# Optimization experiments

Measured on AMD Instinct MI355X. Metric: run time of the kernel, lower is better.

Reference implementation:

```python
import jax, jax.numpy as jnp
import numpy as np

N_HEADS = 16
NEG_BIG = float(-2**32 + 1)  # value the original writes into masked positions


def setup_inputs() -> dict:
    key = jax.random.key(0)
    ks = jax.random.split(key, 5)
    B, T, D = 64, 256, 1024
    s = 1.0 / np.sqrt(D)
    return {
        "x": jax.random.normal(ks[0], (B, T, D), jnp.float32),
        "pos_emb": jax.random.normal(ks[1], (T, D), jnp.float32),
        "Wq": jax.random.normal(ks[2], (D, D), jnp.float32) * s,
        "Wk": jax.random.normal(ks[3], (D, D), jnp.float32) * s,
        "Wv": jax.random.normal(ks[4], (D, D), jnp.float32) * s,
    }


def reference(x, pos_emb, Wq, Wk, Wv):
    B, T, D = x.shape
    H = N_HEADS
    dh = D // H
    # add position embeddings (same arange positions for every batch row)
    temporal = x + pos_emb[None, :T, :]            # [B, T, D]
    q = temporal @ Wq                              # [B, T, D]
    k = temporal @ Wk
    v = temporal @ Wv
    # chunk along feature dim into H heads, concatenate along batch dim -> [H*B, T, dh]
    def split_heads(t):
        return jnp.concatenate(jnp.split(t, H, axis=2), axis=0)
    q_, k_, v_ = split_heads(q), split_heads(k), split_heads(v)
    scores = jnp.einsum('btd,bsd->bts', q_, k_) / jnp.sqrt(jnp.asarray(T, x.dtype))  # [H*B, T, T]
    # original masks the LOWER triangle (tril > 0 -> padding), faithful to source
    tril = jnp.tril(jnp.ones((T, T), x.dtype))
    scores = jnp.where(tril > 0, jnp.asarray(NEG_BIG, x.dtype), scores)
    # original applies softmax over dim=0 (the batch*head axis), faithful to source
    probs = jax.nn.softmax(scores, axis=0)         # [H*B, T, T]
    out = jnp.einsum('bts,bsd->btd', probs, v_)    # [H*B, T, dh]
    # merge heads back: chunk along batch dim, concatenate along feature dim
    out = jnp.concatenate(jnp.split(out, H, axis=0), axis=-1)  # [B, T, D]
    return out
```

## Files before the change

kernel.cpp:

```cpp
#include <hip/hip_runtime.h>

constexpr int SEQ = 256;
constexpr int DIM = 1024;
constexpr float SCALE = 0.0625f;

typedef __attribute__((ext_vector_type(8))) short bf16x8;
typedef __attribute__((ext_vector_type(4))) float f32x4;
typedef unsigned short ushort_t;
typedef unsigned int uint_t;

__device__ __forceinline__ void gld_lds16(const void* g, void* l) {
  __builtin_amdgcn_global_load_lds(
      (const __attribute__((address_space(1))) unsigned int*)g,
      (__attribute__((address_space(3))) unsigned int*)l, 16, 0, 0);
}

__device__ __forceinline__ ushort_t f2bf(float f) {
  uint_t u = __float_as_uint(f);
  return (ushort_t)((u + 0x7fffu + ((u >> 16) & 1u)) >> 16);
}

__device__ __forceinline__ float bf2f(ushort_t h) {
  return __uint_as_float(((uint_t)h) << 16);
}

__global__ __launch_bounds__(256)
void prep_pack(const float* __restrict__ x, const float* __restrict__ pos,
               const float* __restrict__ Wq, const float* __restrict__ Wk,
               const float* __restrict__ Wv,
               ushort_t* __restrict__ Ab, ushort_t* __restrict__ Bp) {
  const int bid = (int)blockIdx.x;
  if (bid < 8192) {
    const size_t idx = ((size_t)bid * 256 + threadIdx.x) * 8;
    const int m = (int)(idx >> 10), k = (int)(idx & 1023);
    float4 x0 = *(const float4*)(x + idx);
    float4 x1 = *(const float4*)(x + idx + 4);
    const float* pp = pos + ((size_t)(m & 255) << 10) + k;
    float4 p0 = *(const float4*)pp;
    float4 p1 = *(const float4*)(pp + 4);
    uint_t w0 = (uint_t)f2bf(x0.x + p0.x) | ((uint_t)f2bf(x0.y + p0.y) << 16);
    uint_t w1 = (uint_t)f2bf(x0.z + p0.z) | ((uint_t)f2bf(x0.w + p0.w) << 16);
    uint_t w2 = (uint_t)f2bf(x1.x + p1.x) | ((uint_t)f2bf(x1.y + p1.y) << 16);
    uint_t w3 = (uint_t)f2bf(x1.z + p1.z) | ((uint_t)f2bf(x1.w + p1.w) << 16);
    *(uint4*)&Ab[idx] = make_uint4(w0, w1, w2, w3);
  } else {
    const int pid = bid - 8192;
    const int z = pid >> 9;
    const int rem = pid & 511;
    const int by = rem >> 2, bx = rem & 3;
    const float* W = (z == 0) ? Wq : (z == 1) ? Wk : Wv;
    const int n  = bx * 256 + threadIdx.x;
    const int k8 = by * 8;
    uint_t h[8];
#pragma unroll
    for (int i = 0; i < 8; ++i) h[i] = f2bf(W[(size_t)(k8 + i) * DIM + n]);
    uint_t hp[4];
#pragma unroll
    for (int j = 0; j < 4; ++j) hp[j] = h[2 * j] | (h[2 * j + 1] << 16);
    const int np = z * 1024 + n;
    const int nb = np >> 8, nl = np & 255;
    const int kc = k8 >> 6, kk = k8 & 63;
    size_t base = (((size_t)nb * 16 + kc) * 256 + nl) * 64 + kk;
    *(uint4*)&Bp[base] = make_uint4(hp[0], hp[1], hp[2], hp[3]);
  }
}

__global__ __launch_bounds__(512, 2)
void qkv_mfma(const ushort_t* __restrict__ Ab, const ushort_t* __restrict__ Bp,
              ushort_t* __restrict__ q_bf, ushort_t* __restrict__ k_bf,
              ushort_t* __restrict__ vT_bf) {
  const int id = (int)blockIdx.x;
  const int q8 = id >> 3;
  const int nb = q8 % 12;
  const int mb = (id & 7) * 8 + q8 / 12;
  const int tid = (int)threadIdx.x;
  const int wave = tid >> 6, lane = tid & 63;
  const int wm = wave >> 2, wn = wave & 3;
  const int l15 = lane & 15, quad = lane >> 4;

  __shared__ ushort_t smem[65536];

  const int r8 = lane >> 3;
  const int lc8 = ((lane & 7) ^ r8) * 8;
  const size_t a_row = ((size_t)(mb * 256 + wave * 8 + r8)) << 10;
  const size_t b_row = ((size_t)((nb * 16) * 256 + wave * 8 + r8)) << 6;
  const int wb = wave * 512;

#define SA(q, tt, c) gld_lds16(Ab + a_row + ((size_t)(q) << 16) + (size_t)(tt) * 64 + lc8, \
                               smem + (c) * 32768 + (q) * 4096 + wb)
#define SB(q, tt, c) gld_lds16(Bp + b_row + (size_t)(tt) * 16384 + (q) * 4096 + lc8, \
                               smem + (c) * 32768 + 16384 + (q) * 4096 + wb)

  const int swz = l15 & 7;
  const int cko0 = (quad ^ swz) * 8;
  const int cko1 = ((4 + quad) ^ swz) * 8;
  const int arow0 = (wm * 128 + l15) * 64;
  const int brow0 = (wn * 64 + l15) * 64;

  f32x4 acc[8][4] = {};
  bf16x8 af[4][2], bf[4][2];

#define LDA_II(IH, ii) do { \
    const int ro = arow0 + ((IH) * 64 + (ii) * 16) * 64; \
    af[ii][0] = *(const bf16x8*)&Ac[ro + cko0]; \
    af[ii][1] = *(const bf16x8*)&Ac[ro + cko1]; } while (0)
#define LDB_J(J) do { const int ro = brow0 + (J) * 1024; \
    bf[J][0] = *(const bf16x8*)&Bc[ro + cko0]; \
    bf[J][1] = *(const bf16x8*)&Bc[ro + cko1]; } while (0)
#define MMQ(IH, II0, II1, J0) do { \
    _Pragma("unroll") for (int ks = 0; ks < 2; ++ks) \
    _Pragma("unroll") for (int ii = (II0); ii < (II1); ++ii) \
    _Pragma("unroll") for (int jj = 0; jj < 2; ++jj) \
      acc[(IH) * 4 + ii][(J0) + jj] = __builtin_amdgcn_mfma_f32_16x16x32_bf16( \
          af[ii][ks], bf[(J0) + jj][ks], acc[(IH) * 4 + ii][(J0) + jj], 0, 0, 0); \
    } while (0)

  SA(0, 0, 0); SA(2, 0, 0); SB(0, 0, 0); SB(1, 0, 0); SB(2, 0, 0); SB(3, 0, 0);
  SA(1, 0, 0); SA(3, 0, 0);
  SB(0, 1, 1); SB(1, 1, 1); SA(0, 1, 1); SA(2, 1, 1);
  asm volatile("s_waitcnt vmcnt(6)" ::: "memory");
  __builtin_amdgcn_s_barrier();

  for (int t = 0; t < 16; ++t) {
    const int cur = t & 1, nxt = cur ^ 1;
    const int tn  = (t < 15) ? t + 1 : 15;
    const int tn2 = (t < 14) ? t + 2 : 15;
    const ushort_t* Ac = &smem[cur * 32768];
    const ushort_t* Bc = Ac + 16384;
    LDA_II(0, 0); LDA_II(0, 1); LDA_II(0, 2); LDA_II(0, 3);
    LDB_J(0); LDB_J(1);
    SB(2, tn, nxt); SB(3, tn, nxt);
    __builtin_amdgcn_s_barrier();
    LDB_J(2); LDB_J(3);
    SA(1, tn, nxt); SA(3, tn, nxt);
    asm volatile("s_waitcnt lgkmcnt(4)" ::: "memory");
    __builtin_amdgcn_s_setprio(1);
    MMQ(0, 0, 4, 0);
    __builtin_amdgcn_s_setprio(0);
    asm volatile("s_waitcnt vmcnt(8)" ::: "memory");
    __builtin_amdgcn_s_barrier();
    asm volatile("s_waitcnt lgkmcnt(0)" ::: "memory");
    __builtin_amdgcn_s_setprio(1);
    MMQ(0, 0, 2, 2);
    __builtin_amdgcn_s_setprio(0);
    LDA_II(1, 0); LDA_II(1, 1);
    __builtin_amdgcn_s_setprio(1);
    MMQ(0, 2, 4, 2);
    __builtin_amdgcn_s_setprio(0);
    LDA_II(1, 2); LDA_II(1, 3);
    __builtin_amdgcn_s_barrier();
    SB(0, tn2, cur); SB(1, tn2, cur);
    asm volatile("s_waitcnt lgkmcnt(0)" ::: "memory");
    __builtin_amdgcn_s_setprio(1);
    MMQ(1, 0, 4, 2);
    __builtin_amdgcn_s_setprio(0);
    __builtin_amdgcn_s_barrier();
    SA(0, tn2, cur); SA(2, tn2, cur);
    __builtin_amdgcn_s_setprio(1);
    MMQ(1, 0, 4, 0);
    __builtin_amdgcn_s_setprio(0);
    asm volatile("s_waitcnt vmcnt(6)" ::: "memory");
    __builtin_amdgcn_s_barrier();
  }

  asm volatile("s_waitcnt vmcnt(0)" ::: "memory");
  const int wq = nb >> 2;
  const int h  = (nb & 3) * 4 + wn;
  if (wq < 2) {
    ushort_t* base = ((wq == 0) ? q_bf : k_bf) + (size_t)(mb * 16 + h) * (SEQ * 64);
    const int tb = wm * 128 + quad * 4;
#pragma unroll
    for (int i = 0; i < 8; ++i)
#pragma unroll
      for (int j = 0; j < 4; ++j) {
        const int d = j * 16 + l15;
#pragma unroll
        for (int r = 0; r < 4; ++r)
          base[(size_t)(tb + i * 16 + r) * 64 + d] = f2bf(acc[i][j][r]);
      }
  } else {
    __builtin_amdgcn_s_barrier();
    ushort_t* L = &smem[wave * 4608];
    ushort_t* vbase = vT_bf + (size_t)(mb * 16 + h) * (64 * SEQ) + wm * 128;
    const int tc = (lane & 7) * 8;
#pragma unroll
    for (int g = 0; g < 2; ++g) {
#pragma unroll
      for (int ii = 0; ii < 4; ++ii)
#pragma unroll
        for (int j = 0; j < 4; ++j) {
          f32x4 v = acc[g * 4 + ii][j];
          uint_t lo = (uint_t)f2bf(v[0]) | ((uint_t)f2bf(v[1]) << 16);
          uint_t hi = (uint_t)f2bf(v[2]) | ((uint_t)f2bf(v[3]) << 16);
          *(uint2*)&L[(j * 16 + l15) * 72 + ii * 16 + quad * 4] = make_uint2(lo, hi);
        }
#pragma unroll
      for (int u = 0; u < 8; ++u) {
        const int d = u * 8 + r8;
        uint4 val = *(const uint4*)&L[d * 72 + tc];
        *(uint4*)&vbase[(size_t)d * SEQ + g * 64 + tc] = val;
      }
    }
  }
#undef SA
#undef SB
#undef LDA_II
#undef LDB_J
#undef MMQ
}

__global__ __launch_bounds__(256)
void stats_mfma(const ushort_t* __restrict__ qb, const ushort_t* __restrict__ kb,
                float* __restrict__ part_l) {
  const int p = blockIdx.x, g = blockIdx.y;
  int tt, ss;
  if (p < 4) { tt = p; ss = p; }
  else {
    const int idx = p - 4;
    tt = (idx < 3) ? 0 : (idx < 5) ? 1 : 2;
    ss = (idx < 3) ? idx + 1 : (idx < 5) ? idx - 1 : 3;
  }
  const bool diag = (p < 4);
  const int tid = threadIdx.x, wave = tid >> 6, lane = tid & 63;
  const int l15 = lane & 15, quad = lane >> 4;

  __shared__ __attribute__((aligned(16))) float red[4][64 * 68];

  f32x4 lacc[4][4] = {};

  for (int i4 = 0; i4 < 8; ++i4) {
    const int bp = g * 32 + wave * 8 + i4;
    const int bh = (bp & 63) * 16 + (bp >> 6);
    const ushort_t* qt = qb + (size_t)bh * (SEQ * 64) + (size_t)(tt * 64) * 64;
    const ushort_t* kt = kb + (size_t)bh * (SEQ * 64) + (size_t)(ss * 64) * 64;
    bf16x8 aq[4][2], bk[4][2];
#pragma unroll
    for (int m = 0; m < 4; ++m)
#pragma unroll
      for (int ks = 0; ks < 2; ++ks) {
        aq[m][ks] = *(const bf16x8*)&qt[(m * 16 + l15) * 64 + ks * 32 + quad * 8];
        bk[m][ks] = *(const bf16x8*)&kt[(m * 16 + l15) * 64 + ks * 32 + quad * 8];
      }
    f32x4 sf[4][4] = {};
#pragma unroll
    for (int ks = 0; ks < 2; ++ks)
#pragma unroll
      for (int m = 0; m < 4; ++m)
#pragma unroll
        for (int n = 0; n < 4; ++n)
          sf[m][n] = __builtin_amdgcn_mfma_f32_16x16x32_bf16(aq[m][ks], bk[n][ks], sf[m][n], 0, 0, 0);
#pragma unroll
    for (int m = 0; m < 4; ++m)
#pragma unroll
      for (int n = 0; n < 4; ++n)
#pragma unroll
        for (int r = 0; r < 4; ++r) {
          float e = __expf(sf[m][n][r] * SCALE);
          if (diag) {
            const int t = tt * 64 + m * 16 + quad * 4 + r;
            const int s = ss * 64 + n * 16 + l15;
            e = (s > t) ? e : 1.0f;
          }
          lacc[m][n][r] += e;
        }
  }
  float* R = red[wave];
#pragma unroll
  for (int m = 0; m < 4; ++m)
#pragma unroll
    for (int r = 0; r < 4; ++r) {
      const int row = m * 16 + quad * 4 + r;
#pragma unroll
      for (int n = 0; n < 4; ++n)
        R[row * 68 + n * 16 + l15] = lacc[m][n][r];
    }
  __syncthreads();
  const int trow = tid >> 2, c0 = (tid & 3) * 16;
  const float* r0 = &red[0][trow * 68 + c0];
  const float* r1 = &red[1][trow * 68 + c0];
  const float* r2 = &red[2][trow * 68 + c0];
  const float* r3 = &red[3][trow * 68 + c0];
  float* pl = part_l + (size_t)g * (SEQ * SEQ) + (size_t)(tt * 64 + trow) * SEQ + ss * 64 + c0;
#pragma unroll
  for (int c = 0; c < 16; c += 4) {
    float4 s0 = *(const float4*)&r0[c];
    float4 s1 = *(const float4*)&r1[c];
    float4 s2 = *(const float4*)&r2[c];
    float4 s3 = *(const float4*)&r3[c];
    float4 o;
    o.x = (s0.x + s1.x) + (s2.x + s3.x);
    o.y = (s0.y + s1.y) + (s2.y + s3.y);
    o.z = (s0.z + s1.z) + (s2.z + s3.z);
    o.w = (s0.w + s1.w) + (s2.w + s3.w);
    *(float4*)&pl[c] = o;
  }
}

__global__ __launch_bounds__(256)
void merge_kernel(const float* __restrict__ part_l, float* __restrict__ inv_lT) {
  const int i = blockIdx.x * 256 + threadIdx.x;
  const int t = i >> 8, s = i & 255;
  float invv;
  if (s <= t) invv = 1.0f / 1024.0f;
  else {
    const float* p = part_l + i;
    float a0 = 0.f, a1 = 0.f, a2 = 0.f, a3 = 0.f,
          a4 = 0.f, a5 = 0.f, a6 = 0.f, a7 = 0.f;
    for (int g = 0; g < 32; g += 8) {
      const float* q = p + ((size_t)g << 16);
      a0 += q[0ull << 16]; a1 += q[1ull << 16]; a2 += q[2ull << 16]; a3 += q[3ull << 16];
      a4 += q[4ull << 16]; a5 += q[5ull << 16]; a6 += q[6ull << 16]; a7 += q[7ull << 16];
    }
    invv = 1.0f / (((a0 + a1) + (a2 + a3)) + ((a4 + a5) + (a6 + a7)));
  }
  inv_lT[s * SEQ + t] = invv;
}

__global__ __launch_bounds__(256)
void pv_mfma(const ushort_t* __restrict__ qb, const ushort_t* __restrict__ kb,
             const ushort_t* __restrict__ vtb, const float* __restrict__ inv_lT,
             float* __restrict__ out) {
  const int bh = blockIdx.x;
  const int b = bh >> 4, h = bh & 15;
  const int tid = threadIdx.x, wave = tid >> 6, lane = tid & 63;
  const int l15 = lane & 15, quad = lane >> 4;
  const int t0 = wave * 64;

  __shared__ ushort_t Plds[4][64][72];
  __shared__ float csumL[4][64];
  ushort_t (*Pw)[72] = Plds[wave];

  const ushort_t* qq = qb + (size_t)bh * (SEQ * 64);
  const ushort_t* kk = kb + (size_t)bh * (SEQ * 64);
  const ushort_t* vv = vtb + (size_t)bh * (64 * SEQ);

  {
    const int d = lane;
    const ushort_t* vr = vv + (size_t)d * SEQ + wave * 64;
    float s = 0.f;
#pragma unroll
    for (int j = 0; j < 8; ++j) {
      bf16x8 v8 = *(const bf16x8*)&vr[j * 8];
#pragma unroll
      for (int e = 0; e < 8; ++e) s += bf2f((ushort_t)v8[e]);
    }
    csumL[wave][d] = s;
  }

  bf16x8 qf[4][2];
#pragma unroll
  for (int nt = 0; nt < 4; ++nt)
#pragma unroll
    for (int ks = 0; ks < 2; ++ks)
      qf[nt][ks] = *(const bf16x8*)&qq[(t0 + nt * 16 + l15) * 64 + ks * 32 + quad * 8];

  __syncthreads();

  f32x4 o[4][4] = {};

  for (int sc = wave; sc < 4; ++sc) {
    bf16x8 kf[4][2];
#pragma unroll
    for (int ms = 0; ms < 4; ++ms)
#pragma unroll
      for (int ks = 0; ks < 2; ++ks)
        kf[ms][ks] = *(const bf16x8*)&kk[(sc * 64 + ms * 16 + l15) * 64 + ks * 32 + quad * 8];
    f32x4 sf[4][4] = {};
#pragma unroll
    for (int ks = 0; ks < 2; ++ks)
#pragma unroll
      for (int ms = 0; ms < 4; ++ms)
#pragma unroll
        for (int nt = 0; nt < 4; ++nt)
          sf[ms][nt] = __builtin_amdgcn_mfma_f32_16x16x32_bf16(kf[ms][ks], qf[nt][ks], sf[ms][nt], 0, 0, 0);
    const bool dg = (sc == wave);
    const int t = t0 + l15;
#pragma unroll
    for (int ms = 0; ms < 4; ++ms)
#pragma unroll
      for (int nt = 0; nt < 4; ++nt) {
        const int sb = sc * 64 + ms * 16 + quad * 4;
        const int tc = t + nt * 16;
        ushort_t pb[4];
#pragma unroll
        for (int r = 0; r < 4; ++r) {
          const int s = sb + r;
          float e = __expf(sf[ms][nt][r] * SCALE);
          if (dg) e = (s > tc) ? e : 1.0f;
          pb[r] = f2bf(e * inv_lT[(size_t)s * SEQ + tc]);
        }
        uint_t lo = (uint_t)pb[0] | ((uint_t)pb[1] << 16);
        uint_t hi = (uint_t)pb[2] | ((uint_t)pb[3] << 16);
        *(uint2*)&Pw[nt * 16 + l15][ms * 16 + quad * 4] = make_uint2(lo, hi);
      }

    bf16x8 vf[4][2], pf[4][2];
#pragma unroll
    for (int nd = 0; nd < 4; ++nd)
#pragma unroll
      for (int ks = 0; ks < 2; ++ks)
        vf[nd][ks] = *(const bf16x8*)&vv[(nd * 16 + l15) * SEQ + sc * 64 + ks * 32 + quad * 8];
#pragma unroll
    for (int mt = 0; mt < 4; ++mt)
#pragma unroll
      for (int ks = 0; ks < 2; ++ks)
        pf[mt][ks] = *(const bf16x8*)&Pw[mt * 16 + l15][ks * 32 + quad * 8];
#pragma unroll
    for (int ks = 0; ks < 2; ++ks)
#pragma unroll
      for (int mt = 0; mt < 4; ++mt)
#pragma unroll
        for (int nd = 0; nd < 4; ++nd)
          o[mt][nd] = __builtin_amdgcn_mfma_f32_16x16x32_bf16(pf[mt][ks], vf[nd][ks], o[mt][nd], 0, 0, 0);
  }

#pragma unroll
  for (int nd = 0; nd < 4; ++nd) {
    const int d = nd * 16 + l15;
    float pref = 0.f;
    for (int w2 = 0; w2 < wave; ++w2) pref += csumL[w2][d];
    const float cc = pref * (1.0f / 1024.0f);
#pragma unroll
    for (int mt = 0; mt < 4; ++mt)
#pragma unroll
      for (int r = 0; r < 4; ++r)
        o[mt][nd][r] += cc;
  }

  float* ob = out + (size_t)b * SEQ * DIM + h * 64;
#pragma unroll
  for (int mt = 0; mt < 4; ++mt)
#pragma unroll
    for (int r = 0; r < 4; ++r) {
      const int t = t0 + mt * 16 + quad * 4 + r;
#pragma unroll
      for (int nd = 0; nd < 4; ++nd)
        ob[(size_t)t * DIM + nd * 16 + l15] = o[mt][nd][r];
    }
}

extern "C" void kernel_launch(void* const* d_in, const int* in_sizes, int n_in,
                              void* d_out, int out_size, void* d_ws, size_t ws_size,
                              hipStream_t stream) {
  const float* x   = (const float*)d_in[0];
  const float* pos = (const float*)d_in[1];
  const float* Wq  = (const float*)d_in[2];
  const float* Wk  = (const float*)d_in[3];
  const float* Wv  = (const float*)d_in[4];
  float* out = (float*)d_out;

  ushort_t* Ab = (ushort_t*)d_out;
  ushort_t* Bp = (ushort_t*)((char*)d_out + 33554432);

  char* W = (char*)d_ws;
  ushort_t* q_bf   = (ushort_t*)(W);
  ushort_t* k_bf   = (ushort_t*)(W + 33554432);
  ushort_t* vT_bf  = (ushort_t*)(W + 67108864);
  float*    part_l = (float*)  (W + 100663296);
  float*    inv_lT = (float*)  (W + 167772160);

  prep_pack<<<dim3(9728), 256, 0, stream>>>(x, pos, Wq, Wk, Wv, Ab, Bp);
  qkv_mfma<<<dim3(768), 512, 0, stream>>>(Ab, Bp, q_bf, k_bf, vT_bf);
  stats_mfma<<<dim3(10, 32), 256, 0, stream>>>(q_bf, k_bf, part_l);
  merge_kernel<<<dim3(SEQ * SEQ / 256), 256, 0, stream>>>(part_l, inv_lT);
  pv_mfma<<<dim3(1024), 256, 0, stream>>>(q_bf, k_bf, vT_bf, inv_lT, out);
}
```

Before: 323.8 us.

## Pair two heads per pv block with reversed wave order; store inv_l untransposed

Each pv_mfma block now handles two (batch, head) pairs. In the second pair the row-block assignment to waves is reversed, so each wave's causal workload is balanced across the two passes (wave w does 4-w plus w+1 tiles). The launch shrinks from 1024 to 512 blocks. The normaliser table is written in row-major t-by-s order so pv can read four consecutive s values as one float4 instead of four strided scalar loads, and the merge kernel's store becomes coalesced. In exchange there are fewer blocks to spread across CUs and the two passes run serially within each block.

```diff
diff --git a/kernel.cpp b/kernel.cpp
--- a/kernel.cpp
+++ b/kernel.cpp
@@ -297,7 +297,7 @@
 }
 
 __global__ __launch_bounds__(256)
-void merge_kernel(const float* __restrict__ part_l, float* __restrict__ inv_lT) {
+void merge_kernel(const float* __restrict__ part_l, float* __restrict__ inv_l) {
   const int i = blockIdx.x * 256 + threadIdx.x;
   const int t = i >> 8, s = i & 255;
   float invv;
@@ -313,30 +313,25 @@
     }
     invv = 1.0f / (((a0 + a1) + (a2 + a3)) + ((a4 + a5) + (a6 + a7)));
   }
-  inv_lT[s * SEQ + t] = invv;
+  inv_l[i] = invv;
 }
 
 __global__ __launch_bounds__(256)
 void pv_mfma(const ushort_t* __restrict__ qb, const ushort_t* __restrict__ kb,
-             const ushort_t* __restrict__ vtb, const float* __restrict__ inv_lT,
+             const ushort_t* __restrict__ vtb, const float* __restrict__ inv_l,
              float* __restrict__ out) {
-  const int bh = blockIdx.x;
-  const int b = bh >> 4, h = bh & 15;
+  const int blk = (int)blockIdx.x;
   const int tid = threadIdx.x, wave = tid >> 6, lane = tid & 63;
   const int l15 = lane & 15, quad = lane >> 4;
-  const int t0 = wave * 64;
 
   __shared__ ushort_t Plds[4][64][72];
-  __shared__ float csumL[4][64];
+  __shared__ float csumL[2][4][64];
   ushort_t (*Pw)[72] = Plds[wave];
 
-  const ushort_t* qq = qb + (size_t)bh * (SEQ * 64);
-  const ushort_t* kk = kb + (size_t)bh * (SEQ * 64);
-  const ushort_t* vv = vtb + (size_t)bh * (64 * SEQ);
-
-  {
-    const int d = lane;
-    const ushort_t* vr = vv + (size_t)d * SEQ + wave * 64;
+#pragma unroll
+  for (int vb = 0; vb < 2; ++vb) {
+    const ushort_t* vr = vtb + (size_t)(blk * 2 + vb) * (64 * SEQ)
+                       + (size_t)lane * SEQ + wave * 64;
     float s = 0.f;
 #pragma unroll
     for (int j = 0; j < 8; ++j) {
@@ -344,99 +339,111 @@
 #pragma unroll
       for (int e = 0; e < 8; ++e) s += bf2f((ushort_t)v8[e]);
     }
-    csumL[wave][d] = s;
-  }
-
-  bf16x8 qf[4][2];
-#pragma unroll
-  for (int nt = 0; nt < 4; ++nt)
-#pragma unroll
-    for (int ks = 0; ks < 2; ++ks)
-      qf[nt][ks] = *(const bf16x8*)&qq[(t0 + nt * 16 + l15) * 64 + ks * 32 + quad * 8];
-
+    csumL[vb][wave][lane] = s;
+  }
   __syncthreads();
 
-  f32x4 o[4][4] = {};
-
-  for (int sc = wave; sc < 4; ++sc) {
-    bf16x8 kf[4][2];
-#pragma unroll
-    for (int ms = 0; ms < 4; ++ms)
+  for (int vb = 0; vb < 2; ++vb) {
+    const int bh = blk * 2 + vb;
+    const int b = bh >> 4, h = bh & 15;
+    const int tb = vb ? (3 - wave) : wave;
+    const int t0 = tb * 64;
+
+    const ushort_t* qq = qb + (size_t)bh * (SEQ * 64);
+    const ushort_t* kk = kb + (size_t)bh * (SEQ * 64);
+    const ushort_t* vv = vtb + (size_t)bh * (64 * SEQ);
+
+    bf16x8 qf[4][2];
+#pragma unroll
+    for (int nt = 0; nt < 4; ++nt)
 #pragma unroll
       for (int ks = 0; ks < 2; ++ks)
-        kf[ms][ks] = *(const bf16x8*)&kk[(sc * 64 + ms * 16 + l15) * 64 + ks * 32 + quad * 8];
-    f32x4 sf[4][4] = {};
-#pragma unroll
-    for (int ks = 0; ks < 2; ++ks)
+        qf[nt][ks] = *(const bf16x8*)&qq[(t0 + nt * 16 + l15) * 64 + ks * 32 + quad * 8];
+
+    f32x4 o[4][4] = {};
+
+    for (int sc = tb; sc < 4; ++sc) {
+      bf16x8 kf[4][2];
 #pragma unroll
       for (int ms = 0; ms < 4; ++ms)
 #pragma unroll
-        for (int nt = 0; nt < 4; ++nt)
-          sf[ms][nt] = __builtin_amdgcn_mfma_f32_16x16x32_bf16(kf[ms][ks], qf[nt][ks], sf[ms][nt], 0, 0, 0);
-    const bool dg = (sc == wave);
-    const int t = t0 + l15;
-#pragma unroll
-    for (int ms = 0; ms < 4; ++ms)
-#pragma unroll
-      for (int nt = 0; nt < 4; ++nt) {
-        const int sb = sc * 64 + ms * 16 + quad * 4;
-        const int tc = t + nt * 16;
-        ushort_t pb[4];
-#pragma unroll
-        for (int r = 0; r < 4; ++r) {
-          const int s = sb + r;
-          float e = __expf(sf[ms][nt][r] * SCALE);
-          if (dg) e = (s > tc) ? e : 1.0f;
-          pb[r] = f2bf(e * inv_lT[(size_t)s * SEQ + tc]);
+        for (int ks = 0; ks < 2; ++ks)
+          kf[ms][ks] = *(const bf16x8*)&kk[(sc * 64 + ms * 16 + l15) * 64 + ks * 32 + quad * 8];
+      f32x4 sf[4][4] = {};
+#pragma unroll
+      for (int ks = 0; ks < 2; ++ks)
+#pragma unroll
+        for (int ms = 0; ms < 4; ++ms)
+#pragma unroll
+          for (int nt = 0; nt < 4; ++nt)
+            sf[ms][nt] = __builtin_amdgcn_mfma_f32_16x16x32_bf16(kf[ms][ks], qf[nt][ks], sf[ms][nt], 0, 0, 0);
+      const bool dg = (sc == tb);
+      const int t = t0 + l15;
+#pragma unroll
+      for (int ms = 0; ms < 4; ++ms)
+#pragma unroll
+        for (int nt = 0; nt < 4; ++nt) {
+          const int sb = sc * 64 + ms * 16 + quad * 4;
+          const int tc = t + nt * 16;
+          const float4 iv = *(const float4*)&inv_l[(size_t)tc * SEQ + sb];
+          ushort_t pb[4];
+#pragma unroll
+          for (int r = 0; r < 4; ++r) {
+            const int s = sb + r;
+            float e = __expf(sf[ms][nt][r] * SCALE);
+            if (dg) e = (s > tc) ? e : 1.0f;
+            const float ivr = (r == 0) ? iv.x : (r == 1) ? iv.y : (r == 2) ? iv.z : iv.w;
+            pb[r] = f2bf(e * ivr);
+          }
+          uint_t lo = (uint_t)pb[0] | ((uint_t)pb[1] << 16);
+          uint_t hi = (uint_t)pb[2] | ((uint_t)pb[3] << 16);
+          *(uint2*)&Pw[nt * 16 + l15][ms * 16 + quad * 4] = make_uint2(lo, hi);
         }
-        uint_t lo = (uint_t)pb[0] | ((uint_t)pb[1] << 16);
-        uint_t hi = (uint_t)pb[2] | ((uint_t)pb[3] << 16);
-        *(uint2*)&Pw[nt * 16 + l15][ms * 16 + quad * 4] = make_uint2(lo, hi);
+
+      bf16x8 vf[4][2], pf[4][2];
+#pragma unroll
+      for (int nd = 0; nd < 4; ++nd)
+#pragma unroll
+        for (int ks = 0; ks < 2; ++ks)
+          vf[nd][ks] = *(const bf16x8*)&vv[(nd * 16 + l15) * SEQ + sc * 64 + ks * 32 + quad * 8];
+#pragma unroll
+      for (int mt = 0; mt < 4; ++mt)
+#pragma unroll
+        for (int ks = 0; ks < 2; ++ks)
+          pf[mt][ks] = *(const bf16x8*)&Pw[mt * 16 + l15][ks * 32 + quad * 8];
+#pragma unroll
+      for (int ks = 0; ks < 2; ++ks)
+#pragma unroll
+        for (int mt = 0; mt < 4; ++mt)
+#pragma unroll
+          for (int nd = 0; nd < 4; ++nd)
+            o[mt][nd] = __builtin_amdgcn_mfma_f32_16x16x32_bf16(pf[mt][ks], vf[nd][ks], o[mt][nd], 0, 0, 0);
+    }
+
+#pragma unroll
+    for (int nd = 0; nd < 4; ++nd) {
+      const int d = nd * 16 + l15;
+      float pref = 0.f;
+      for (int w2 = 0; w2 < tb; ++w2) pref += csumL[vb][w2][d];
+      const float cc = pref * (1.0f / 1024.0f);
+#pragma unroll
+      for (int mt = 0; mt < 4; ++mt)
+#pragma unroll
+        for (int r = 0; r < 4; ++r)
+          o[mt][nd][r] += cc;
+    }
+
+    float* ob = out + (size_t)b * SEQ * DIM + h * 64;
+#pragma unroll
+    for (int mt = 0; mt < 4; ++mt)
+#pragma unroll
+      for (int r = 0; r < 4; ++r) {
+        const int t = t0 + mt * 16 + quad * 4 + r;
+#pragma unroll
+        for (int nd = 0; nd < 4; ++nd)
+          ob[(size_t)t * DIM + nd * 16 + l15] = o[mt][nd][r];
       }
-
-    bf16x8 vf[4][2], pf[4][2];
-#pragma unroll
-    for (int nd = 0; nd < 4; ++nd)
-#pragma unroll
-      for (int ks = 0; ks < 2; ++ks)
-        vf[nd][ks] = *(const bf16x8*)&vv[(nd * 16 + l15) * SEQ + sc * 64 + ks * 32 + quad * 8];
-#pragma unroll
-    for (int mt = 0; mt < 4; ++mt)
-#pragma unroll
-      for (int ks = 0; ks < 2; ++ks)
-        pf[mt][ks] = *(const bf16x8*)&Pw[mt * 16 + l15][ks * 32 + quad * 8];
-#pragma unroll
-    for (int ks = 0; ks < 2; ++ks)
-#pragma unroll
-      for (int mt = 0; mt < 4; ++mt)
-#pragma unroll
-        for (int nd = 0; nd < 4; ++nd)
-          o[mt][nd] = __builtin_amdgcn_mfma_f32_16x16x32_bf16(pf[mt][ks], vf[nd][ks], o[mt][nd], 0, 0, 0);
-  }
-
-#pragma unroll
-  for (int nd = 0; nd < 4; ++nd) {
-    const int d = nd * 16 + l15;
-    float pref = 0.f;
-    for (int w2 = 0; w2 < wave; ++w2) pref += csumL[w2][d];
-    const float cc = pref * (1.0f / 1024.0f);
-#pragma unroll
-    for (int mt = 0; mt < 4; ++mt)
-#pragma unroll
-      for (int r = 0; r < 4; ++r)
-        o[mt][nd][r] += cc;
-  }
-
-  float* ob = out + (size_t)b * SEQ * DIM + h * 64;
-#pragma unroll
-  for (int mt = 0; mt < 4; ++mt)
-#pragma unroll
-    for (int r = 0; r < 4; ++r) {
-      const int t = t0 + mt * 16 + quad * 4 + r;
-#pragma unroll
-      for (int nd = 0; nd < 4; ++nd)
-        ob[(size_t)t * DIM + nd * 16 + l15] = o[mt][nd][r];
-    }
+  }
 }
 
 extern "C" void kernel_launch(void* const* d_in, const int* in_sizes, int n_in,
@@ -457,11 +464,11 @@
   ushort_t* k_bf   = (ushort_t*)(W + 33554432);
   ushort_t* vT_bf  = (ushort_t*)(W + 67108864);
   float*    part_l = (float*)  (W + 100663296);
-  float*    inv_lT = (float*)  (W + 167772160);
+  float*    inv_l  = (float*)  (W + 167772160);
 
   prep_pack<<<dim3(9728), 256, 0, stream>>>(x, pos, Wq, Wk, Wv, Ab, Bp);
   qkv_mfma<<<dim3(768), 512, 0, stream>>>(Ab, Bp, q_bf, k_bf, vT_bf);
   stats_mfma<<<dim3(10, 32), 256, 0, stream>>>(q_bf, k_bf, part_l);
-  merge_kernel<<<dim3(SEQ * SEQ / 256), 256, 0, stream>>>(part_l, inv_lT);
-  pv_mfma<<<dim3(1024), 256, 0, stream>>>(q_bf, k_bf, vT_bf, inv_lT, out);
-}
+  merge_kernel<<<dim3(SEQ * SEQ / 256), 256, 0, stream>>>(part_l, inv_l);
+  pv_mfma<<<dim3(512), 256, 0, stream>>>(q_bf, k_bf, vT_bf, inv_l, out);
+}
```

After: 321.0 us. Within noise of the previous version (-0.9%).
